# Kernel tuning notes

Hardware: AMD Instinct MI355X
Metric: run time of the kernel (lower is better)

Reference implementation:

```python
import jax, jax.numpy as jnp
import numpy as np

N_NODES = 100000
N_EDGES = 1600000
D = 128
BETA = 0.001
EPS = 1e-12  # F.normalize eps


def setup_inputs() -> dict:
    key = jax.random.key(0)
    k1, k2, k3, k4, k5, k6 = jax.random.split(key, 6)
    stdv = 1.0 / np.sqrt(D)
    return {
        "input": jax.random.normal(k1, (N_NODES, D), dtype=jnp.float32),
        "edge_rows": jax.random.randint(k2, (N_EDGES,), 0, N_NODES, dtype=jnp.int32),
        "edge_cols": jax.random.randint(k3, (N_EDGES,), 0, N_NODES, dtype=jnp.int32),
        "edge_vals": jax.random.uniform(k4, (N_EDGES,), dtype=jnp.float32),
        "weight": jax.random.uniform(k5, (D, D), minval=-stdv, maxval=stdv, dtype=jnp.float32),
        "bias": jax.random.uniform(k6, (D,), minval=-stdv, maxval=stdv, dtype=jnp.float32),
    }


def reference(input, edge_rows, edge_cols, edge_vals, weight, bias):
    # dense projection: [N, D]
    support = input @ weight
    # sparse neighbor aggregation: agg[i] = sum_{(i,j) in E} adj_val * support[j]
    msgs = edge_vals[:, None] * support[edge_cols]          # [E, D]
    agg = jax.ops.segment_sum(msgs, edge_rows, num_segments=input.shape[0])
    # beta-weighted residual blend
    out = BETA * input + (1.0 - BETA) * agg
    # row-wise L2 normalize (torch F.normalize, p=2, dim=1)
    norm = jnp.sqrt(jnp.sum(out * out, axis=1, keepdims=True))
    out = out / jnp.maximum(norm, EPS)
    # bias add
    return out + bias
```

## Files before the change

### kernel.cpp

```cpp
#include <hip/hip_runtime.h>

#define N_NODES 100000
#define N_EDGES 1600000
#define D 128
#define NB 1563
#define NSUB 8
#define SUBCAP 224
#define CAP (NSUB*SUBCAP)

typedef short bf16x8 __attribute__((ext_vector_type(8)));
typedef float f32x4 __attribute__((ext_vector_type(4)));

__device__ __forceinline__ unsigned short f2bf(float x){
  union { float f; unsigned u; } v; v.f = x;
  unsigned r = v.u + 0x7fffu + ((v.u >> 16) & 1u);
  return (unsigned short)(r >> 16);
}

__device__ __forceinline__ float bf2f(unsigned short h){
  union { unsigned u; float f; } v; v.u = ((unsigned)h) << 16;
  return v.f;
}

__global__ __launch_bounds__(256) void convert_input(const float4* __restrict__ in4,
                                                     ushort4* __restrict__ outb,
                                                     int* __restrict__ cursor,
                                                     const float* __restrict__ W,
                                                     unsigned short* __restrict__ WT){
  int i = blockIdx.x*256 + threadIdx.x;
  if (i < NSUB*NB) cursor[i] = 0;
  if (i < D*D){
    int k = i >> 7, c = i & 127;
    WT[c*128 + k] = f2bf(W[i]);
  }
  float4 a = in4[i];
  ushort4 h;
  h.x = f2bf(a.x); h.y = f2bf(a.y); h.z = f2bf(a.z); h.w = f2bf(a.w);
  outb[i] = h;
}

__global__ __launch_bounds__(256) void scatter_direct(const int* __restrict__ rows,
                                                      const int* __restrict__ cols,
                                                      const float* __restrict__ vals,
                                                      int* __restrict__ cursor,
                                                      int2* __restrict__ edges_s){
  int i = blockIdx.x*256 + threadIdx.x;
  int s = blockIdx.x & (NSUB-1);
  int r = rows[i];
  int b = r >> 6;
  int pos = atomicAdd(&cursor[s*NB + b], 1);
  if (pos < SUBCAP)
    edges_s[(size_t)b*CAP + s*SUBCAP + pos] =
        make_int2(cols[i] | ((r & 63) << 17), __float_as_int(vals[i]));
}

__global__ __launch_bounds__(512) void agg_final(const ushort4* __restrict__ inb4,
                                                 const int* __restrict__ cursor,
                                                 const int2* __restrict__ edges_g,
                                                 const unsigned short* __restrict__ WTg,
                                                 const float* __restrict__ bias,
                                                 float* __restrict__ out){
  __shared__ __align__(16) unsigned char pool[64*136*2];
  __shared__ unsigned short As[64*136];
  __shared__ int hist[64];
  __shared__ int cur[64];
  __shared__ int rs[64];
  __shared__ int rc[64];
  __shared__ float rsum[2][64];
  __shared__ int rowctr;
  int2* st = (int2*)pool;
  unsigned short* Bs = (unsigned short*)pool;

  int t = threadIdx.x;
  int b = blockIdx.x;
  size_t base = (size_t)b * CAP;

  if (t < 64) hist[t] = 0;
  if (t == 0) rowctr = 0;
  __syncthreads();

  int2 held[NSUB];
  int hv = 0;
  #pragma unroll
  for (int s = 0; s < NSUB; ++s){
    int ms = cursor[s*NB + b];
    if (ms > SUBCAP) ms = SUBCAP;
    if (t < ms){
      int2 e = edges_g[base + s*SUBCAP + t];
      held[s] = e;
      hv |= (1 << s);
      atomicAdd(&hist[((unsigned)e.x) >> 17], 1);
    }
  }
  __syncthreads();

  if (t < 64){
    int c = hist[t];
    int x = c;
    #pragma unroll
    for (int o = 1; o < 64; o <<= 1){
      int y = __shfl_up(x, o);
      if (t >= o) x += y;
    }
    int excl = x - c;
    cur[t] = excl;
    rs[t] = excl;
    rc[t] = c;
  }
  __syncthreads();

  #pragma unroll
  for (int s = 0; s < NSUB; ++s){
    if (hv & (1 << s)){
      int2 e = held[s];
      int r = ((unsigned)e.x) >> 17;
      int pos = atomicAdd(&cur[r], 1);
      st[pos] = make_int2(e.x & 0x1FFFF, e.y);
    }
  }
  __syncthreads();

  int l = t & 31;
  for (;;){
    int r = 0;
    if (l == 0) r = atomicAdd(&rowctr, 1);
    r = __shfl(r, 0, 32);
    if (r >= 64) break;

    int e = rs[r], end = e + rc[r];
    float4 a0 = make_float4(0.f,0.f,0.f,0.f);
    float4 a1 = make_float4(0.f,0.f,0.f,0.f);
    float4 a2 = make_float4(0.f,0.f,0.f,0.f);
    float4 a3 = make_float4(0.f,0.f,0.f,0.f);
    for (; e + 4 <= end; e += 4){
      int2 e0 = st[e+0];
      int2 e1 = st[e+1];
      int2 e2 = st[e+2];
      int2 e3 = st[e+3];
      ushort4 x0 = inb4[(size_t)e0.x*32 + l];
      ushort4 x1 = inb4[(size_t)e1.x*32 + l];
      ushort4 x2 = inb4[(size_t)e2.x*32 + l];
      ushort4 x3 = inb4[(size_t)e3.x*32 + l];
      float v0 = __int_as_float(e0.y), v1 = __int_as_float(e1.y);
      float v2 = __int_as_float(e2.y), v3 = __int_as_float(e3.y);
      a0.x = fmaf(v0, bf2f(x0.x), a0.x); a0.y = fmaf(v0, bf2f(x0.y), a0.y);
      a0.z = fmaf(v0, bf2f(x0.z), a0.z); a0.w = fmaf(v0, bf2f(x0.w), a0.w);
      a1.x = fmaf(v1, bf2f(x1.x), a1.x); a1.y = fmaf(v1, bf2f(x1.y), a1.y);
      a1.z = fmaf(v1, bf2f(x1.z), a1.z); a1.w = fmaf(v1, bf2f(x1.w), a1.w);
      a2.x = fmaf(v2, bf2f(x2.x), a2.x); a2.y = fmaf(v2, bf2f(x2.y), a2.y);
      a2.z = fmaf(v2, bf2f(x2.z), a2.z); a2.w = fmaf(v2, bf2f(x2.w), a2.w);
      a3.x = fmaf(v3, bf2f(x3.x), a3.x); a3.y = fmaf(v3, bf2f(x3.y), a3.y);
      a3.z = fmaf(v3, bf2f(x3.z), a3.z); a3.w = fmaf(v3, bf2f(x3.w), a3.w);
    }
    for (; e < end; ++e){
      int2 ee = st[e];
      ushort4 x = inb4[(size_t)ee.x*32 + l];
      float v = __int_as_float(ee.y);
      a0.x = fmaf(v, bf2f(x.x), a0.x); a0.y = fmaf(v, bf2f(x.y), a0.y);
      a0.z = fmaf(v, bf2f(x.z), a0.z); a0.w = fmaf(v, bf2f(x.w), a0.w);
    }
    float4 sres;
    sres.x = (a0.x + a1.x) + (a2.x + a3.x);
    sres.y = (a0.y + a1.y) + (a2.y + a3.y);
    sres.z = (a0.z + a1.z) + (a2.z + a3.z);
    sres.w = (a0.w + a1.w) + (a2.w + a3.w);
    ushort4 h;
    h.x = f2bf(sres.x); h.y = f2bf(sres.y);
    h.z = f2bf(sres.z); h.w = f2bf(sres.w);
    *((ushort4*)&As[r*136 + l*4]) = h;
  }
  __syncthreads();

  int w = t >> 6, lane = t & 63;
  int wr = w >> 1, wc = w & 1;
  int q = lane >> 4, n = lane & 15;
  int block_row = b * 64;

  #pragma unroll
  for (int i = 0; i < 4; ++i){
    int idx4 = i*512 + t;
    int row = idx4 >> 5, k4 = idx4 & 31;
    int grow = block_row + row;
    ushort4 h = make_ushort4(0,0,0,0);
    if (grow < N_NODES) h = inb4[(size_t)grow*32 + k4];
    *((ushort4*)&Bs[row*136 + k4*4]) = h;
  }

  bf16x8 afr[4];
  #pragma unroll
  for (int ks = 0; ks < 4; ++ks)
    afr[ks] = *((const bf16x8*)&As[(wr*16 + n)*136 + ks*32 + q*8]);

  f32x4 acc[4];
  #pragma unroll
  for (int ct = 0; ct < 4; ++ct) acc[ct] = (f32x4){0.f, 0.f, 0.f, 0.f};
  #pragma unroll
  for (int ct = 0; ct < 4; ++ct){
    #pragma unroll
    for (int ks = 0; ks < 4; ++ks){
      bf16x8 bfr = *((const bf16x8*)(WTg + (wc*64 + ct*16 + n)*128 + ks*32 + q*8));
      acc[ct] = __builtin_amdgcn_mfma_f32_16x16x32_bf16(afr[ks], bfr, acc[ct], 0, 0, 0);
    }
  }
  __syncthreads();

  float v[4][4];
  float s[4] = {0.f, 0.f, 0.f, 0.f};
  #pragma unroll
  for (int reg = 0; reg < 4; ++reg){
    int row_local = wr*16 + q*4 + reg;
    #pragma unroll
    for (int ct = 0; ct < 4; ++ct){
      float inp = bf2f(Bs[row_local*136 + wc*64 + ct*16 + n]);
      float val = fmaf(0.999f, acc[ct][reg], 0.001f * inp);
      v[ct][reg] = val;
      s[reg] = fmaf(val, val, s[reg]);
    }
  }
  #pragma unroll
  for (int reg = 0; reg < 4; ++reg){
    float x = s[reg];
    x += __shfl_xor(x, 1);
    x += __shfl_xor(x, 2);
    x += __shfl_xor(x, 4);
    x += __shfl_xor(x, 8);
    s[reg] = x;
  }
  if (n == 0){
    #pragma unroll
    for (int reg = 0; reg < 4; ++reg)
      rsum[wc][wr*16 + q*4 + reg] = s[reg];
  }
  __syncthreads();

  #pragma unroll
  for (int reg = 0; reg < 4; ++reg){
    int row_local = wr*16 + q*4 + reg;
    int grow = block_row + row_local;
    if (grow >= N_NODES) continue;
    float tot = rsum[0][row_local] + rsum[1][row_local];
    float scale = 1.f / fmaxf(sqrtf(tot), 1e-12f);
    float* outrow = out + (size_t)grow * D;
    #pragma unroll
    for (int ct = 0; ct < 4; ++ct){
      int c = wc*64 + ct*16 + n;
      outrow[c] = fmaf(v[ct][reg], scale, bias[c]);
    }
  }
}

extern "C" void kernel_launch(void* const* d_in, const int* in_sizes, int n_in,
                              void* d_out, int out_size, void* d_ws, size_t ws_size,
                              hipStream_t stream){
  const float* input  = (const float*)d_in[0];
  const int*   erows  = (const int*)d_in[1];
  const int*   ecols  = (const int*)d_in[2];
  const float* evals  = (const float*)d_in[3];
  const float* weight = (const float*)d_in[4];
  const float* bias   = (const float*)d_in[5];
  float* out = (float*)d_out;

  int*   cursor    = (int*)d_ws;
  int2*  edges_s   = (int2*)(cursor + NSUB*NB);
  ushort4* inb     = (ushort4*)(edges_s + (size_t)NB*CAP);
  unsigned short* WTg = (unsigned short*)(inb + (size_t)N_NODES * 32);

  convert_input<<<12500, 256, 0, stream>>>((const float4*)input, inb, cursor, weight, WTg);
  scatter_direct<<<N_EDGES/256, 256, 0, stream>>>(erows, ecols, evals, cursor, edges_s);
  agg_final<<<NB, 512, 0, stream>>>((const ushort4*)inb, cursor, edges_s,
                                    WTg, bias, out);
}
```

Measured before the change: 306.5 us.

## Bin edges by column slice so blocks gather from a shared source window

Edges in each 64-row block are now binned by source-column slice (8 slices of 12500 nodes) as well as by destination row. Each 32-lane group owns 4 fixed rows and walks the slices in lockstep, with a block barrier after each slice. The aim is that concurrent blocks read gathered rows from the same region of the source table at the same time, which should improve cache locality. In exchange it adds masked FMAs (4x the arithmetic per edge), 8 barriers, static row assignment that can be load-imbalanced, and a larger scan.

```diff
diff --git a/kernel.cpp b/kernel.cpp
--- a/kernel.cpp
+++ b/kernel.cpp
@@ -7,6 +7,8 @@
 #define NSUB 8
 #define SUBCAP 224
 #define CAP (NSUB*SUBCAP)
+#define NSLICE 8
+#define SLICE_W 12500
 
 typedef short bf16x8 __attribute__((ext_vector_type(8)));
 typedef float f32x4 __attribute__((ext_vector_type(4)));
@@ -62,12 +64,10 @@
                                                  float* __restrict__ out){
   __shared__ __align__(16) unsigned char pool[64*136*2];
   __shared__ unsigned short As[64*136];
-  __shared__ int hist[64];
-  __shared__ int cur[64];
-  __shared__ int rs[64];
-  __shared__ int rc[64];
+  __shared__ int rs[NSLICE*64 + 1];
+  __shared__ int cur[NSLICE*64];
+  __shared__ int wsum[8];
   __shared__ float rsum[2][64];
-  __shared__ int rowctr;
   int2* st = (int2*)pool;
   unsigned short* Bs = (unsigned short*)pool;
 
@@ -75,8 +75,7 @@
   int b = blockIdx.x;
   size_t base = (size_t)b * CAP;
 
-  if (t < 64) hist[t] = 0;
-  if (t == 0) rowctr = 0;
+  cur[t] = 0;
   __syncthreads();
 
   int2 held[NSUB];
@@ -89,23 +88,32 @@
       int2 e = edges_g[base + s*SUBCAP + t];
       held[s] = e;
       hv |= (1 << s);
-      atomicAdd(&hist[((unsigned)e.x) >> 17], 1);
-    }
-  }
-  __syncthreads();
-
-  if (t < 64){
-    int c = hist[t];
+      int col = e.x & 0x1FFFF;
+      int bin = (col / SLICE_W)*64 + (((unsigned)e.x) >> 17);
+      atomicAdd(&cur[bin], 1);
+    }
+  }
+  __syncthreads();
+
+  {
+    int c = cur[t];
+    int w = t >> 6, lane = t & 63;
     int x = c;
     #pragma unroll
     for (int o = 1; o < 64; o <<= 1){
       int y = __shfl_up(x, o);
-      if (t >= o) x += y;
-    }
-    int excl = x - c;
+      if (lane >= o) x += y;
+    }
+    if (lane == 63) wsum[w] = x;
+    __syncthreads();
+    int pre = 0;
+    #pragma unroll
+    for (int ww = 0; ww < 8; ++ww)
+      if (ww < w) pre += wsum[ww];
+    int excl = pre + x - c;
+    rs[t] = excl;
     cur[t] = excl;
-    rs[t] = excl;
-    rc[t] = c;
+    if (t == 511) rs[512] = excl + c;
   }
   __syncthreads();
 
@@ -113,61 +121,65 @@
   for (int s = 0; s < NSUB; ++s){
     if (hv & (1 << s)){
       int2 e = held[s];
-      int r = ((unsigned)e.x) >> 17;
-      int pos = atomicAdd(&cur[r], 1);
-      st[pos] = make_int2(e.x & 0x1FFFF, e.y);
-    }
-  }
-  __syncthreads();
-
-  int l = t & 31;
-  for (;;){
-    int r = 0;
-    if (l == 0) r = atomicAdd(&rowctr, 1);
-    r = __shfl(r, 0, 32);
-    if (r >= 64) break;
-
-    int e = rs[r], end = e + rc[r];
-    float4 a0 = make_float4(0.f,0.f,0.f,0.f);
-    float4 a1 = make_float4(0.f,0.f,0.f,0.f);
-    float4 a2 = make_float4(0.f,0.f,0.f,0.f);
-    float4 a3 = make_float4(0.f,0.f,0.f,0.f);
+      int col = e.x & 0x1FFFF;
+      int bin = (col / SLICE_W)*64 + (((unsigned)e.x) >> 17);
+      int pos = atomicAdd(&cur[bin], 1);
+      st[pos] = e;
+    }
+  }
+  __syncthreads();
+
+  int grp = t >> 5, l = t & 31;
+  float4 r0 = make_float4(0.f,0.f,0.f,0.f);
+  float4 r1 = make_float4(0.f,0.f,0.f,0.f);
+  float4 r2 = make_float4(0.f,0.f,0.f,0.f);
+  float4 r3 = make_float4(0.f,0.f,0.f,0.f);
+
+#define EDGE_ACC(E) { \
+    int col_ = (E).x & 0x1FFFF; \
+    int j_ = (((unsigned)(E).x) >> 17) & 3; \
+    float v_ = __int_as_float((E).y); \
+    ushort4 X_ = inb4[(size_t)col_*32 + l]; \
+    float f0_ = (j_==0)? v_ : 0.f; \
+    float f1_ = (j_==1)? v_ : 0.f; \
+    float f2_ = (j_==2)? v_ : 0.f; \
+    float f3_ = (j_==3)? v_ : 0.f; \
+    float xx_ = bf2f(X_.x), xy_ = bf2f(X_.y), xz_ = bf2f(X_.z), xw_ = bf2f(X_.w); \
+    r0.x = fmaf(f0_, xx_, r0.x); r0.y = fmaf(f0_, xy_, r0.y); \
+    r0.z = fmaf(f0_, xz_, r0.z); r0.w = fmaf(f0_, xw_, r0.w); \
+    r1.x = fmaf(f1_, xx_, r1.x); r1.y = fmaf(f1_, xy_, r1.y); \
+    r1.z = fmaf(f1_, xz_, r1.z); r1.w = fmaf(f1_, xw_, r1.w); \
+    r2.x = fmaf(f2_, xx_, r2.x); r2.y = fmaf(f2_, xy_, r2.y); \
+    r2.z = fmaf(f2_, xz_, r2.z); r2.w = fmaf(f2_, xw_, r2.w); \
+    r3.x = fmaf(f3_, xx_, r3.x); r3.y = fmaf(f3_, xy_, r3.y); \
+    r3.z = fmaf(f3_, xz_, r3.z); r3.w = fmaf(f3_, xw_, r3.w); }
+
+  for (int s = 0; s < NSLICE; ++s){
+    int bin0 = (s << 6) + (grp << 2);
+    int e = rs[bin0];
+    int end = rs[bin0 + 4];
     for (; e + 4 <= end; e += 4){
-      int2 e0 = st[e+0];
-      int2 e1 = st[e+1];
-      int2 e2 = st[e+2];
-      int2 e3 = st[e+3];
-      ushort4 x0 = inb4[(size_t)e0.x*32 + l];
-      ushort4 x1 = inb4[(size_t)e1.x*32 + l];
-      ushort4 x2 = inb4[(size_t)e2.x*32 + l];
-      ushort4 x3 = inb4[(size_t)e3.x*32 + l];
-      float v0 = __int_as_float(e0.y), v1 = __int_as_float(e1.y);
-      float v2 = __int_as_float(e2.y), v3 = __int_as_float(e3.y);
-      a0.x = fmaf(v0, bf2f(x0.x), a0.x); a0.y = fmaf(v0, bf2f(x0.y), a0.y);
-      a0.z = fmaf(v0, bf2f(x0.z), a0.z); a0.w = fmaf(v0, bf2f(x0.w), a0.w);
-      a1.x = fmaf(v1, bf2f(x1.x), a1.x); a1.y = fmaf(v1, bf2f(x1.y), a1.y);
-      a1.z = fmaf(v1, bf2f(x1.z), a1.z); a1.w = fmaf(v1, bf2f(x1.w), a1.w);
-      a2.x = fmaf(v2, bf2f(x2.x), a2.x); a2.y = fmaf(v2, bf2f(x2.y), a2.y);
-      a2.z = fmaf(v2, bf2f(x2.z), a2.z); a2.w = fmaf(v2, bf2f(x2.w), a2.w);
-      a3.x = fmaf(v3, bf2f(x3.x), a3.x); a3.y = fmaf(v3, bf2f(x3.y), a3.y);
-      a3.z = fmaf(v3, bf2f(x3.z), a3.z); a3.w = fmaf(v3, bf2f(x3.w), a3.w);
+      int2 E0 = st[e+0], E1 = st[e+1], E2 = st[e+2], E3 = st[e+3];
+      EDGE_ACC(E0); EDGE_ACC(E1); EDGE_ACC(E2); EDGE_ACC(E3);
     }
     for (; e < end; ++e){
-      int2 ee = st[e];
-      ushort4 x = inb4[(size_t)ee.x*32 + l];
-      float v = __int_as_float(ee.y);
-      a0.x = fmaf(v, bf2f(x.x), a0.x); a0.y = fmaf(v, bf2f(x.y), a0.y);
-      a0.z = fmaf(v, bf2f(x.z), a0.z); a0.w = fmaf(v, bf2f(x.w), a0.w);
-    }
-    float4 sres;
-    sres.x = (a0.x + a1.x) + (a2.x + a3.x);
-    sres.y = (a0.y + a1.y) + (a2.y + a3.y);
-    sres.z = (a0.z + a1.z) + (a2.z + a3.z);
-    sres.w = (a0.w + a1.w) + (a2.w + a3.w);
+      int2 E = st[e];
+      EDGE_ACC(E);
+    }
+    __syncthreads();
+  }
+#undef EDGE_ACC
+
+  {
     ushort4 h;
-    h.x = f2bf(sres.x); h.y = f2bf(sres.y);
-    h.z = f2bf(sres.z); h.w = f2bf(sres.w);
-    *((ushort4*)&As[r*136 + l*4]) = h;
+    h.x = f2bf(r0.x); h.y = f2bf(r0.y); h.z = f2bf(r0.z); h.w = f2bf(r0.w);
+    *((ushort4*)&As[(grp*4+0)*136 + l*4]) = h;
+    h.x = f2bf(r1.x); h.y = f2bf(r1.y); h.z = f2bf(r1.z); h.w = f2bf(r1.w);
+    *((ushort4*)&As[(grp*4+1)*136 + l*4]) = h;
+    h.x = f2bf(r2.x); h.y = f2bf(r2.y); h.z = f2bf(r2.z); h.w = f2bf(r2.w);
+    *((ushort4*)&As[(grp*4+2)*136 + l*4]) = h;
+    h.x = f2bf(r3.x); h.y = f2bf(r3.y); h.z = f2bf(r3.z); h.w = f2bf(r3.w);
+    *((ushort4*)&As[(grp*4+3)*136 + l*4]) = h;
   }
   __syncthreads();
 
```

Result: no change. 308.4 us (+0.6%).
